# Kernel tuning notes

Measured on AMD Instinct MI355X. Metric: run time of the kernel, lower is better.

## Reference

```python
import jax, jax.numpy as jnp
import numpy as np

B, T, C = 2, 2048, 768
N_HEADS = 12
D_K = C // N_HEADS  # 64


def setup_inputs() -> dict:
    key = jax.random.key(0)
    k1, k2, k3, k4, k5 = jax.random.split(key, 5)
    x = jax.random.normal(k1, (B, T, C), dtype=jnp.float32)
    # glorot-normal-ish scaled params
    query_mat = jax.random.normal(k2, (C, N_HEADS, D_K), dtype=jnp.float32) * (2.0 / (C + D_K)) ** 0.5
    key_mat = jax.random.normal(k3, (C, N_HEADS, D_K), dtype=jnp.float32) * (2.0 / (C + D_K)) ** 0.5
    value_mat = jax.random.normal(k4, (C, N_HEADS, D_K), dtype=jnp.float32) * (2.0 / (C + D_K)) ** 0.5
    linear_m1 = jax.random.normal(k5, (C, C), dtype=jnp.float32) * (2.0 / (C + C)) ** 0.5
    return {"x": x, "query_mat": query_mat, "key_mat": key_mat,
            "value_mat": value_mat, "linear_m1": linear_m1}


def reference(x, query_mat, key_mat, value_mat, linear_m1):
    b, t, c = x.shape
    h, d_k = query_mat.shape[1], query_mat.shape[2]
    q = jnp.einsum('btc,chd->bhtd', x, query_mat)
    k = jnp.einsum('btc,chd->bhtd', x, key_mat)
    v = jnp.einsum('btc,chd->bhtd', x, value_mat)
    # NOTE: original module MULTIPLIES by sqrt(d_k) (not divides) - kept faithful.
    w = jnp.einsum('bhtd,bhzd->bhtz', q, k) * (d_k ** 0.5)
    causal = jnp.tril(jnp.ones((t, t), dtype=bool))  # [T,T], True on/below diag
    w = jnp.where(causal, w, -jnp.inf)
    w = jax.nn.softmax(w, axis=-1)
    o = jnp.einsum('bhtz,bhzd->bhtd', w, v)
    o = jnp.transpose(o, (0, 2, 1, 3)).reshape(b, t, h * d_k)
    return jnp.einsum('btc,cz->btz', o, linear_m1)
```

## Files before the change

kernel.cpp:

```cpp
#include <hip/hip_runtime.h>
#include <hip/hip_bf16.h>


typedef float f32x4 __attribute__((ext_vector_type(4)));
typedef short s16x8 __attribute__((ext_vector_type(8)));

#define MFMA(a, b, c) __builtin_amdgcn_mfma_f32_16x16x32_bf16((a), (b), (c), 0, 0, 0)

constexpr int Bb = 2, Tt = 2048, Cc = 768, Hh = 12, Dd = 64;
constexpr int Mm = Bb * Tt;
constexpr int BH = Bb * Hh;

__device__ __forceinline__ void gload16(const void* g, void* l) {
  __builtin_amdgcn_global_load_lds((const __attribute__((address_space(1))) void*)g,
                                   (__attribute__((address_space(3))) void*)l, 16, 0, 0);
}

__device__ __forceinline__ short f2bfbits(float f) {
  __hip_bfloat16 h = __float2bfloat16(f);
  return __builtin_bit_cast(short, h);
}
__device__ __forceinline__ float bf2f(short s) {
  __hip_bfloat16 h = __builtin_bit_cast(__hip_bfloat16, s);
  return __bfloat162float(h);
}
__device__ __forceinline__ unsigned int packbf2(float a, float b) {
  return (unsigned int)(unsigned short)f2bfbits(a) |
         ((unsigned int)(unsigned short)f2bfbits(b) << 16);
}

__global__ __launch_bounds__(256) void prep_all(
    const float* __restrict__ x,
    const float* __restrict__ s0, const float* __restrict__ s1,
    const float* __restrict__ s2, const float* __restrict__ s3,
    __hip_bfloat16* __restrict__ xhi, __hip_bfloat16* __restrict__ xlo,
    __hip_bfloat16* __restrict__ h0, __hip_bfloat16* __restrict__ l0,
    __hip_bfloat16* __restrict__ h1, __hip_bfloat16* __restrict__ l1,
    __hip_bfloat16* __restrict__ h2, __hip_bfloat16* __restrict__ h3) {
  __shared__ float tile[64][65];
  const int bid = blockIdx.x;
  if (bid < 1536) {
    const size_t i = ((size_t)bid * 256 + threadIdx.x) * 8;
    float4 a = *reinterpret_cast<const float4*>(x + i);
    float4 b = *reinterpret_cast<const float4*>(x + i + 4);
    float v[8] = {a.x, a.y, a.z, a.w, b.x, b.y, b.z, b.w};
    s16x8 hi, lo;
#pragma unroll
    for (int j = 0; j < 8; ++j) {
      short h = f2bfbits(v[j]);
      hi[j] = h;
      lo[j] = f2bfbits(v[j] - bf2f(h));
    }
    *reinterpret_cast<s16x8*>((short*)xhi + i) = hi;
    *reinterpret_cast<s16x8*>((short*)xlo + i) = lo;
    return;
  }
  const int q = bid - 1536;
  const int z = q / 144, rem = q % 144;
  const int by = rem / 12, bx = rem % 12;
  const float* src;
  __hip_bfloat16 *dh, *dl = nullptr;
  switch (z) {
    case 0: src = s0; dh = h0; dl = l0; break;
    case 1: src = s1; dh = h1; dl = l1; break;
    case 2: src = s2; dh = h2; break;
    default: src = s3; dh = h3; break;
  }
  const int r0 = by * 64, c0 = bx * 64;
  const int tid = threadIdx.x;
  const int rr = tid >> 4, c4 = (tid & 15) * 4;
#pragma unroll
  for (int it = 0; it < 4; ++it) {
    float4 v = *reinterpret_cast<const float4*>(src + (size_t)(r0 + rr + it * 16) * Cc + c0 + c4);
    tile[rr + it * 16][c4 + 0] = v.x;
    tile[rr + it * 16][c4 + 1] = v.y;
    tile[rr + it * 16][c4 + 2] = v.z;
    tile[rr + it * 16][c4 + 3] = v.w;
  }
  __syncthreads();
#pragma unroll
  for (int it = 0; it < 2; ++it) {
    const int id = tid + it * 256;
    const int n = id >> 3, ch = (id & 7) * 8;
    s16x8 hi, lo;
#pragma unroll
    for (int j = 0; j < 8; ++j) {
      float v = tile[ch + j][n];
      short h = f2bfbits(v);
      hi[j] = h;
      lo[j] = f2bfbits(v - bf2f(h));
    }
    *reinterpret_cast<s16x8*>(dh + (size_t)(c0 + n) * Cc + r0 + ch) = hi;
    if (dl) *reinterpret_cast<s16x8*>(dl + (size_t)(c0 + n) * Cc + r0 + ch) = lo;
  }
}

__device__ __forceinline__ void gemm128_core(const __hip_bfloat16* __restrict__ A,
                                             const __hip_bfloat16* __restrict__ Bt,
                                             int m0, int n0,
                                             short* ldsA, short* ldsB,
                                             f32x4 acc[4][4]) {
  const int tid = threadIdx.x;
  const int w = tid >> 6, l = tid & 63;
  const int wr = w >> 1, wc = w & 1;
  const int srow = l >> 2;
  const int scol = (l & 3) << 3;

  for (int kt = 0; kt < Cc / 32; ++kt) {
    const int kk = kt << 5;
#pragma unroll
    for (int i = 0; i < 2; ++i) {
      const int r = (w << 5) + (i << 4);
      gload16(A + (size_t)(m0 + r + srow) * Cc + kk + scol, ldsA + r * 32);
      gload16(Bt + (size_t)(n0 + r + srow) * Cc + kk + scol, ldsB + r * 32);
    }
    __syncthreads();
    s16x8 af[4], bfr[4];
#pragma unroll
    for (int i = 0; i < 4; ++i) {
      af[i]  = *reinterpret_cast<const s16x8*>(ldsA + ((wr << 6) + (i << 4) + (l & 15)) * 32 + ((l >> 4) << 3));
      bfr[i] = *reinterpret_cast<const s16x8*>(ldsB + ((wc << 6) + (i << 4) + (l & 15)) * 32 + ((l >> 4) << 3));
    }
#pragma unroll
    for (int i = 0; i < 4; ++i)
#pragma unroll
      for (int j = 0; j < 4; ++j)
        acc[i][j] = MFMA(af[i], bfr[j], acc[i][j]);
    __syncthreads();
  }
}

__device__ __forceinline__ void gemm128_hilo(
    const __hip_bfloat16* __restrict__ Ahi, const __hip_bfloat16* __restrict__ Alo,
    const __hip_bfloat16* __restrict__ Bhi, const __hip_bfloat16* __restrict__ Blo,
    bool lo, int m0, int n0, short* lds, f32x4 acc[4][4]) {
  short* ldsAh = lds;
  short* ldsAl = lds + 4096;
  short* ldsBh = lds + 8192;
  short* ldsBl = lds + 12288;
  const int tid = threadIdx.x;
  const int w = tid >> 6, l = tid & 63;
  const int wr = w >> 1, wc = w & 1;
  const int srow = l >> 2;
  const int scol = (l & 3) << 3;

  for (int kt = 0; kt < Cc / 32; ++kt) {
    const int kk = kt << 5;
#pragma unroll
    for (int i = 0; i < 2; ++i) {
      const int r = (w << 5) + (i << 4);
      const size_t aoff = (size_t)(m0 + r + srow) * Cc + kk + scol;
      const size_t boff = (size_t)(n0 + r + srow) * Cc + kk + scol;
      gload16(Ahi + aoff, ldsAh + r * 32);
      gload16(Bhi + boff, ldsBh + r * 32);
      if (lo) {
        gload16(Alo + aoff, ldsAl + r * 32);
        gload16(Blo + boff, ldsBl + r * 32);
      }
    }
    __syncthreads();
    s16x8 ah[4], bh[4], al[4], bl[4];
#pragma unroll
    for (int i = 0; i < 4; ++i) {
      const int ao = ((wr << 6) + (i << 4) + (l & 15)) * 32 + ((l >> 4) << 3);
      const int bo = ((wc << 6) + (i << 4) + (l & 15)) * 32 + ((l >> 4) << 3);
      ah[i] = *reinterpret_cast<const s16x8*>(ldsAh + ao);
      bh[i] = *reinterpret_cast<const s16x8*>(ldsBh + bo);
      if (lo) {
        al[i] = *reinterpret_cast<const s16x8*>(ldsAl + ao);
        bl[i] = *reinterpret_cast<const s16x8*>(ldsBl + bo);
      }
    }
#pragma unroll
    for (int i = 0; i < 4; ++i)
#pragma unroll
      for (int j = 0; j < 4; ++j)
        acc[i][j] = MFMA(ah[i], bh[j], acc[i][j]);
    if (lo) {
#pragma unroll
      for (int i = 0; i < 4; ++i)
#pragma unroll
        for (int j = 0; j < 4; ++j) {
          acc[i][j] = MFMA(ah[i], bl[j], acc[i][j]);
          acc[i][j] = MFMA(al[i], bh[j], acc[i][j]);
        }
    }
    __syncthreads();
  }
}

__global__ __launch_bounds__(256) void qkv_gemm(
    const __hip_bfloat16* __restrict__ Xhi, const __hip_bfloat16* __restrict__ Xlo,
    const __hip_bfloat16* __restrict__ WqThi, const __hip_bfloat16* __restrict__ WqTlo,
    const __hip_bfloat16* __restrict__ WkThi, const __hip_bfloat16* __restrict__ WkTlo,
    const __hip_bfloat16* __restrict__ WvThi,
    __hip_bfloat16* __restrict__ Qhi, __hip_bfloat16* __restrict__ Qlo,
    __hip_bfloat16* __restrict__ Khi, __hip_bfloat16* __restrict__ Klo,
    __hip_bfloat16* __restrict__ V) {
  __shared__ __align__(16) short lds[16384];
  const int z = blockIdx.z;
  const bool lo = (z < 2);
  const __hip_bfloat16* Bhi = (z == 0) ? WqThi : (z == 1) ? WkThi : WvThi;
  const __hip_bfloat16* Blo = (z == 0) ? WqTlo : WkTlo;
  const int m0 = blockIdx.x * 128, n0 = blockIdx.y * 128;

  f32x4 acc[4][4];
#pragma unroll
  for (int i = 0; i < 4; ++i)
#pragma unroll
    for (int j = 0; j < 4; ++j) acc[i][j] = f32x4{0.f, 0.f, 0.f, 0.f};

  gemm128_hilo(Xhi, Xlo, Bhi, Blo, lo, m0, n0, lds, acc);

  const int tid = threadIdx.x, w = tid >> 6, l = tid & 63;
  const int wr = w >> 1, wc = w & 1;
#pragma unroll
  for (int i = 0; i < 4; ++i) {
#pragma unroll
    for (int j = 0; j < 4; ++j) {
#pragma unroll
      for (int r = 0; r < 4; ++r) {
        const int m = m0 + (wr << 6) + (i << 4) + ((l >> 4) << 2) + r;
        const int n = n0 + (wc << 6) + (j << 4) + (l & 15);
        float v = acc[i][j][r];
        const int b = m >> 11, t = m & 2047, h = n >> 6, d = n & 63;
        const size_t idx = (((size_t)(b * Hh + h)) * Tt + t) * Dd + d;
        if (z == 2) {
          V[idx] = __float2bfloat16(v);
        } else {
          if (z == 0) v *= 8.0f;
          short hbits = f2bfbits(v);
          short lbits = f2bfbits(v - bf2f(hbits));
          if (z == 0) { ((short*)Qhi)[idx] = hbits; ((short*)Qlo)[idx] = lbits; }
          else        { ((short*)Khi)[idx] = hbits; ((short*)Klo)[idx] = lbits; }
        }
      }
    }
  }
}

__global__ __launch_bounds__(256) void proj_gemm(
    const __hip_bfloat16* __restrict__ O, const __hip_bfloat16* __restrict__ LT,
    float* __restrict__ out) {
  __shared__ __align__(16) short lds[8192];
  const int m0 = blockIdx.x * 128, n0 = blockIdx.y * 128;
  f32x4 acc[4][4];
#pragma unroll
  for (int i = 0; i < 4; ++i)
#pragma unroll
    for (int j = 0; j < 4; ++j) acc[i][j] = f32x4{0.f, 0.f, 0.f, 0.f};

  gemm128_core(O, LT, m0, n0, lds, lds + 4096, acc);

  const int tid = threadIdx.x, w = tid >> 6, l = tid & 63;
  const int wr = w >> 1, wc = w & 1;
#pragma unroll
  for (int i = 0; i < 4; ++i)
#pragma unroll
    for (int j = 0; j < 4; ++j)
#pragma unroll
      for (int r = 0; r < 4; ++r) {
        const int m = m0 + (wr << 6) + (i << 4) + ((l >> 4) << 2) + r;
        const int n = n0 + (wc << 6) + (j << 4) + (l & 15);
        out[(size_t)m * Cc + n] = acc[i][j][r];
      }
}

__global__ __launch_bounds__(256) void transpose_v(
    const __hip_bfloat16* __restrict__ V, __hip_bfloat16* __restrict__ VT) {
  __shared__ __align__(16) short tile[64][72];
  const int t0 = blockIdx.x * 64, bh = blockIdx.y;
  const __hip_bfloat16* src = V + (size_t)bh * Tt * Dd;
  __hip_bfloat16* dst = VT + (size_t)bh * Dd * Tt;
  const int tid = threadIdx.x;
  const int rr = tid >> 3;
  const int cc = (tid & 7) << 3;
#pragma unroll
  for (int it = 0; it < 2; ++it) {
    const int r = rr + it * 32;
    *reinterpret_cast<s16x8*>(&tile[r][cc]) =
        *reinterpret_cast<const s16x8*>(src + (size_t)(t0 + r) * Dd + cc);
  }
  __syncthreads();
#pragma unroll
  for (int it = 0; it < 2; ++it) {
    const int d = rr + it * 32;
    s16x8 o;
#pragma unroll
    for (int j = 0; j < 8; ++j) o[j] = tile[cc + j][d];
    *reinterpret_cast<s16x8*>(dst + (size_t)d * Tt + t0 + cc) = o;
  }
}

__global__ __launch_bounds__(256, 3) void attn_fwd(
    const __hip_bfloat16* __restrict__ Qhi, const __hip_bfloat16* __restrict__ Qlo,
    const __hip_bfloat16* __restrict__ Khi, const __hip_bfloat16* __restrict__ Klo,
    const __hip_bfloat16* __restrict__ VT, __hip_bfloat16* __restrict__ O) {
  __shared__ __align__(16) short kvk[2][2][4096];
  __shared__ __align__(16) short kvv[4096];
  __shared__ __align__(16) short pbuf[4][16 * 72];
  const int i = blockIdx.x;
  const int j = i >> 3;
  const int m3 = j >> 5;
  const int bh = (i & 7) * 3 + m3;
  const int sp = ((j & 31) + 11 * m3) & 31;
  const int qblk = (sp & 1) ? (sp >> 1) : (31 - (sp >> 1));
  const int b = bh / Hh, h = bh % Hh;
  const int tid = threadIdx.x, w = tid >> 6, l = tid & 63;
  const int lr = l & 15, lg = l >> 4;
  const int q0 = qblk * 64 + w * 16;
  const size_t hqk = (size_t)bh * Tt * Dd;
  const __hip_bfloat16* qhp = Qhi + hqk;
  const __hip_bfloat16* qlp = Qlo + hqk;
  const __hip_bfloat16* khp = Khi + hqk;
  const __hip_bfloat16* klp = Klo + hqk;
  const __hip_bfloat16* vtp = VT + (size_t)bh * Dd * Tt;
  short* myP = &pbuf[w][0];
  short* obase = (short*)O + (size_t)b * Tt * Cc + h * Dd;

  const int rr = l >> 3;
  const int gg = (l & 7) ^ rr;

  auto stageK = [&](int buf, int k0) {
#pragma unroll
    for (int s6 = 0; s6 < 4; ++s6) {
      const int s = w * 4 + s6;
      const int m = s >> 3, i2 = s & 7;
      const int row = i2 * 8 + rr;
      const __hip_bfloat16* src = (m == 0)
          ? khp + (size_t)(k0 + row) * Dd + gg * 8
          : klp + (size_t)(k0 + row) * Dd + gg * 8;
      gload16(src, &kvk[buf][m][i2 * 512]);
    }
  };
  auto stageV = [&](int k0) {
#pragma unroll
    for (int s6 = 0; s6 < 2; ++s6) {
      const int i2 = w * 2 + s6;
      const int row = i2 * 8 + rr;
      gload16(vtp + (size_t)row * Tt + k0 + gg * 8, &kvv[i2 * 512]);
    }
  };

  stageK(0, 0);
  stageV(0);

  s16x8 qh[2], ql[2];
#pragma unroll
  for (int df = 0; df < 2; ++df) {
    const size_t off = (size_t)(q0 + lr) * Dd + df * 32 + lg * 8;
    qh[df] = *reinterpret_cast<const s16x8*>(qhp + off);
    ql[df] = *reinterpret_cast<const s16x8*>(qlp + off);
  }

  f32x4 oacc[4];
#pragma unroll
  for (int df = 0; df < 4; ++df) oacc[df] = f32x4{0.f, 0.f, 0.f, 0.f};
  float mrow = -__builtin_inff(), lrow = 0.f;

  __syncthreads();

  const int sw = lr & 7;
  const int nt = qblk;
  for (int kt = 0; kt <= nt; ++kt) {
    const int cur = kt & 1;
    const int k0 = kt << 6;
    if (kt > 0) stageV(k0);
    if (kt < nt) stageK(cur ^ 1, (kt + 1) << 6);

    const short* Kh = &kvk[cur][0][0];
    const short* Kl = &kvk[cur][1][0];

    f32x4 s[4];
#pragma unroll
    for (int kjf = 0; kjf < 4; ++kjf) s[kjf] = f32x4{0.f, 0.f, 0.f, 0.f};
#pragma unroll
    for (int kjf = 0; kjf < 4; ++kjf)
#pragma unroll
      for (int df = 0; df < 2; ++df) {
        const int off = (kjf * 16 + lr) * 64 + (((df * 4 + lg) ^ sw) << 3);
        const s16x8 kh = *reinterpret_cast<const s16x8*>(Kh + off);
        const s16x8 kl = *reinterpret_cast<const s16x8*>(Kl + off);
        s[kjf] = MFMA(kh, qh[df], s[kjf]);
        s[kjf] = MFMA(kl, qh[df], s[kjf]);
        s[kjf] = MFMA(kh, ql[df], s[kjf]);
      }

    const int q = q0 + lr;
    const bool dotmask = (k0 + 63) > q0;
    float mx = -__builtin_inff();
#pragma unroll
    for (int kjf = 0; kjf < 4; ++kjf)
#pragma unroll
      for (int r = 0; r < 4; ++r) {
        float v = s[kjf][r];
        if (dotmask && (k0 + kjf * 16 + lg * 4 + r) > q) v = -__builtin_inff();
        s[kjf][r] = v;
        mx = fmaxf(mx, v);
      }
    mx = fmaxf(mx, __shfl_xor(mx, 16));
    mx = fmaxf(mx, __shfl_xor(mx, 32));
    const float mnew = fmaxf(mrow, mx);
    const float sc = __expf(mrow - mnew);
    mrow = mnew;
    float ls = 0.f;
#pragma unroll
    for (int kjf = 0; kjf < 4; ++kjf)
#pragma unroll
      for (int r = 0; r < 4; ++r) {
        const float p = __expf(s[kjf][r] - mnew);
        s[kjf][r] = p;
        ls += p;
      }
    ls += __shfl_xor(ls, 16);
    ls += __shfl_xor(ls, 32);
    lrow = lrow * sc + ls;
#pragma unroll
    for (int df = 0; df < 4; ++df) oacc[df] *= sc;

#pragma unroll
    for (int kjf = 0; kjf < 4; ++kjf) {
      uint2 pk;
      pk.x = packbf2(s[kjf][0], s[kjf][1]);
      pk.y = packbf2(s[kjf][2], s[kjf][3]);
      *reinterpret_cast<uint2*>(myP + lr * 72 + kjf * 16 + lg * 4) = pk;
    }

    if (kt < nt) {
      asm volatile("s_waitcnt vmcnt(4)" ::: "memory");
    } else {
      asm volatile("s_waitcnt vmcnt(0)" ::: "memory");
    }
    __builtin_amdgcn_sched_barrier(0);

#pragma unroll
    for (int kf = 0; kf < 2; ++kf) {
      const s16x8 pa = *reinterpret_cast<const s16x8*>(myP + lr * 72 + kf * 32 + lg * 8);
#pragma unroll
      for (int df = 0; df < 4; ++df) {
        const int off = (df * 16 + lr) * 64 + (((kf * 4 + lg) ^ sw) << 3);
        const s16x8 bv = *reinterpret_cast<const s16x8*>(kvv + off);
        oacc[df] = MFMA(bv, pa, oacc[df]);
      }
    }

    __syncthreads();
  }

  const float inv = 1.0f / lrow;
  const int t = q0 + lr;
#pragma unroll
  for (int df = 0; df < 4; ++df) {
    uint2 pk;
    pk.x = packbf2(oacc[df][0] * inv, oacc[df][1] * inv);
    pk.y = packbf2(oacc[df][2] * inv, oacc[df][3] * inv);
    *reinterpret_cast<uint2*>(obase + (size_t)t * Cc + df * 16 + lg * 4) = pk;
  }
}

extern "C" void kernel_launch(void* const* d_in, const int* in_sizes, int n_in,
                              void* d_out, int out_size, void* d_ws, size_t ws_size,
                              hipStream_t stream) {
  (void)in_sizes; (void)n_in; (void)out_size; (void)ws_size;
  const float* x  = (const float*)d_in[0];
  const float* wq = (const float*)d_in[1];
  const float* wk = (const float*)d_in[2];
  const float* wv = (const float*)d_in[3];
  const float* lm = (const float*)d_in[4];
  float* out = (float*)d_out;
  __hip_bfloat16* ws = (__hip_bfloat16*)d_ws;

  const size_t WSZ = (size_t)Cc * Cc;
  const size_t TSZ = (size_t)Mm * Cc;
  __hip_bfloat16* WqThi = ws;
  __hip_bfloat16* WqTlo = WqThi + WSZ;
  __hip_bfloat16* WkThi = WqTlo + WSZ;
  __hip_bfloat16* WkTlo = WkThi + WSZ;
  __hip_bfloat16* WvThi = WkTlo + WSZ;
  __hip_bfloat16* LThi  = WvThi + WSZ;
  __hip_bfloat16* Xhi   = LThi + WSZ;
  __hip_bfloat16* Xlo   = Xhi + TSZ;
  __hip_bfloat16* Qhi   = Xlo + TSZ;
  __hip_bfloat16* Qlo   = Qhi + TSZ;
  __hip_bfloat16* Khi   = Qlo + TSZ;
  __hip_bfloat16* Klo   = Khi + TSZ;
  __hip_bfloat16* Vb    = Klo + TSZ;
  __hip_bfloat16* VT    = Vb + TSZ;
  __hip_bfloat16* Ob    = Vb;

  prep_all<<<dim3(2112), 256, 0, stream>>>(x, wq, wk, wv, lm, Xhi, Xlo,
                                           WqThi, WqTlo, WkThi, WkTlo, WvThi, LThi);
  qkv_gemm<<<dim3(32, 6, 3), 256, 0, stream>>>(Xhi, Xlo, WqThi, WqTlo, WkThi, WkTlo,
                                               WvThi, Qhi, Qlo, Khi, Klo, Vb);
  transpose_v<<<dim3(32, BH), 256, 0, stream>>>(Vb, VT);
  attn_fwd<<<dim3(768), 256, 0, stream>>>(Qhi, Qlo, Khi, Klo, VT, Ob);
  proj_gemm<<<dim3(32, 6), 256, 0, stream>>>(Ob, LThi, out);
}
```

Before: 133.5 us.

## Write V transposed from QKV GEMM epilogue and rebalance attention block schedule

The V output of the QKV GEMM is now stored directly in transposed [bh][d][t] layout, with four consecutive t values packed into one 8-byte store. This removes the separate transpose_v kernel launch and its extra read/write pass over V. The attention kernel's mapping from block index to query block also changes from a parity-interleaved formula to a set of lookup-table permutations. The aim is to balance causal work across concurrently resident blocks, though the tables add a little index arithmetic per block.

```diff
diff --git a/kernel.cpp b/kernel.cpp
--- a/kernel.cpp
+++ b/kernel.cpp
@@ -196,7 +196,7 @@
     const __hip_bfloat16* __restrict__ WvThi,
     __hip_bfloat16* __restrict__ Qhi, __hip_bfloat16* __restrict__ Qlo,
     __hip_bfloat16* __restrict__ Khi, __hip_bfloat16* __restrict__ Klo,
-    __hip_bfloat16* __restrict__ V) {
+    __hip_bfloat16* __restrict__ VT) {
   __shared__ __align__(16) short lds[16384];
   const int z = blockIdx.z;
   const bool lo = (z < 2);
@@ -214,6 +214,22 @@
 
   const int tid = threadIdx.x, w = tid >> 6, l = tid & 63;
   const int wr = w >> 1, wc = w & 1;
+  if (z == 2) {
+#pragma unroll
+    for (int i = 0; i < 4; ++i)
+#pragma unroll
+      for (int j = 0; j < 4; ++j) {
+        const int mb = m0 + (wr << 6) + (i << 4) + ((l >> 4) << 2);
+        const int n = n0 + (wc << 6) + (j << 4) + (l & 15);
+        const int b = mb >> 11, t0 = mb & 2047, h = n >> 6, d = n & 63;
+        uint2 pk;
+        pk.x = packbf2(acc[i][j][0], acc[i][j][1]);
+        pk.y = packbf2(acc[i][j][2], acc[i][j][3]);
+        *reinterpret_cast<uint2*>(
+            (short*)VT + ((size_t)(b * Hh + h) * Dd + d) * Tt + t0) = pk;
+      }
+    return;
+  }
 #pragma unroll
   for (int i = 0; i < 4; ++i) {
 #pragma unroll
@@ -225,15 +241,11 @@
         float v = acc[i][j][r];
         const int b = m >> 11, t = m & 2047, h = n >> 6, d = n & 63;
         const size_t idx = (((size_t)(b * Hh + h)) * Tt + t) * Dd + d;
-        if (z == 2) {
-          V[idx] = __float2bfloat16(v);
-        } else {
-          if (z == 0) v *= 8.0f;
-          short hbits = f2bfbits(v);
-          short lbits = f2bfbits(v - bf2f(hbits));
-          if (z == 0) { ((short*)Qhi)[idx] = hbits; ((short*)Qlo)[idx] = lbits; }
-          else        { ((short*)Khi)[idx] = hbits; ((short*)Klo)[idx] = lbits; }
-        }
+        if (z == 0) v *= 8.0f;
+        short hbits = f2bfbits(v);
+        short lbits = f2bfbits(v - bf2f(hbits));
+        if (z == 0) { ((short*)Qhi)[idx] = hbits; ((short*)Qlo)[idx] = lbits; }
+        else        { ((short*)Khi)[idx] = hbits; ((short*)Klo)[idx] = lbits; }
       }
     }
   }
@@ -264,32 +276,6 @@
         const int n = n0 + (wc << 6) + (j << 4) + (l & 15);
         out[(size_t)m * Cc + n] = acc[i][j][r];
       }
-}
-
-__global__ __launch_bounds__(256) void transpose_v(
-    const __hip_bfloat16* __restrict__ V, __hip_bfloat16* __restrict__ VT) {
-  __shared__ __align__(16) short tile[64][72];
-  const int t0 = blockIdx.x * 64, bh = blockIdx.y;
-  const __hip_bfloat16* src = V + (size_t)bh * Tt * Dd;
-  __hip_bfloat16* dst = VT + (size_t)bh * Dd * Tt;
-  const int tid = threadIdx.x;
-  const int rr = tid >> 3;
-  const int cc = (tid & 7) << 3;
-#pragma unroll
-  for (int it = 0; it < 2; ++it) {
-    const int r = rr + it * 32;
-    *reinterpret_cast<s16x8*>(&tile[r][cc]) =
-        *reinterpret_cast<const s16x8*>(src + (size_t)(t0 + r) * Dd + cc);
-  }
-  __syncthreads();
-#pragma unroll
-  for (int it = 0; it < 2; ++it) {
-    const int d = rr + it * 32;
-    s16x8 o;
-#pragma unroll
-    for (int j = 0; j < 8; ++j) o[j] = tile[cc + j][d];
-    *reinterpret_cast<s16x8*>(dst + (size_t)d * Tt + t0 + cc) = o;
-  }
 }
 
 __global__ __launch_bounds__(256, 3) void attn_fwd(
@@ -303,8 +289,14 @@
   const int j = i >> 3;
   const int m3 = j >> 5;
   const int bh = (i & 7) * 3 + m3;
-  const int sp = ((j & 31) + 11 * m3) & 31;
-  const int qblk = (sp & 1) ? (sp >> 1) : (31 - (sp >> 1));
+  const int s_ = j & 31;
+  const int h1t[8] = {3, 4, 7, 5, 2, 6, 1, 0};
+  const int h2t[8] = {7, 6, 1, 2, 5, 0, 3, 4};
+  const int p1t[4] = {2, 3, 1, 0};
+  const int p2t[4] = {3, 0, 2, 1};
+  const int qblk = (m3 == 0) ? s_
+                 : (m3 == 1) ? 4 * h1t[s_ >> 2] + p1t[s_ & 3]
+                             : 4 * h2t[s_ >> 2] + p2t[s_ & 3];
   const int b = bh / Hh, h = bh % Hh;
   const int tid = threadIdx.x, w = tid >> 6, l = tid & 63;
   const int lr = l & 15, lg = l >> 4;
@@ -491,8 +483,7 @@
   prep_all<<<dim3(2112), 256, 0, stream>>>(x, wq, wk, wv, lm, Xhi, Xlo,
                                            WqThi, WqTlo, WkThi, WkTlo, WvThi, LThi);
   qkv_gemm<<<dim3(32, 6, 3), 256, 0, stream>>>(Xhi, Xlo, WqThi, WqTlo, WkThi, WkTlo,
-                                               WvThi, Qhi, Qlo, Khi, Klo, Vb);
-  transpose_v<<<dim3(32, BH), 256, 0, stream>>>(Vb, VT);
+                                               WvThi, Qhi, Qlo, Khi, Klo, VT);
   attn_fwd<<<dim3(768), 256, 0, stream>>>(Qhi, Qlo, Khi, Klo, VT, Ob);
   proj_gemm<<<dim3(32, 6), 256, 0, stream>>>(Ob, LThi, out);
 }
```

New measurement: 120.4 us. 1.11x faster.
